# Performance work log

Hardware: AMD Instinct MI355X
Metric: run time of the kernel (lower is better)

The kernel has to match this reference:

```python
import jax, jax.numpy as jnp
import numpy as np

B, L, D, N_ITEMS, HEADS = 32, 1024, 1024, 50000, 2


def setup_inputs() -> dict:
    key = jax.random.key(0)
    ks = jax.random.split(key, 14)
    positives = jax.random.randint(ks[0], (B, L), 0, N_ITEMS)
    mask = jax.random.randint(ks[1], (B, L), 0, 2).astype(jnp.int32)
    s = 0.02
    item_emb = jax.random.normal(ks[2], (N_ITEMS + 1, D), jnp.float32) * s
    pos_emb = jax.random.normal(ks[3], (L, D), jnp.float32) * s
    Wz = jax.random.normal(ks[4], (L, L), jnp.float32) * s
    Wv = jax.random.normal(ks[5], (L, L), jnp.float32) * s
    Wq = jax.random.normal(ks[6], (L, L), jnp.float32) * s
    Wk = jax.random.normal(ks[7], (L, L), jnp.float32) * s
    gamma_q = jax.random.normal(ks[8], (HEADS, L), jnp.float32) * s
    beta_q = jnp.zeros((HEADS, L), jnp.float32)
    gamma_k = jax.random.normal(ks[9], (HEADS, L), jnp.float32) * s
    beta_k = jnp.zeros((HEADS, L), jnp.float32)
    sparse_w = jax.random.uniform(ks[10], (L, L), jnp.float32)
    return {"positives": positives, "mask": mask, "item_emb": item_emb,
            "pos_emb": pos_emb, "Wz": Wz, "Wv": Wv, "Wq": Wq, "Wk": Wk,
            "gamma_q": gamma_q, "beta_q": beta_q, "gamma_k": gamma_k,
            "beta_k": beta_k, "sparse_w": sparse_w}


def _merge_attn_masks(mask):
    # True == not allowed to attend
    pad = ~(mask.astype(bool))[:, None, :]                 # (B,1,L)
    future = jnp.triu(jnp.ones((L, L), bool), k=1)         # (L,L)
    merged = pad | future[None]                             # (B,L,L)
    diag = ~jnp.eye(L, dtype=bool)
    return diag[None] & merged                              # (B,L,L) bool


def reference(positives, mask, item_emb, pos_emb, Wz, Wv, Wq, Wk,
              gamma_q, beta_q, gamma_k, beta_k, sparse_w):
    attn_mask = _merge_attn_masks(mask)                     # (B,L,L) bool
    x = item_emb[positives] + pos_emb[None]                 # (B,L,D)
    # encoder
    z = jax.nn.silu(jnp.einsum('bld,ed->ble', x, Wz))       # (B,L,L-dim feats)
    zq = jnp.einsum('bld,ed->ble', z, Wq)
    zk = jnp.einsum('bld,ed->ble', z, Wk)
    q = zq * gamma_q[0] + beta_q[0]                         # head 0 only
    k = zk * gamma_k[0] + beta_k[0]
    a = jnp.einsum('bqd,bkd->bqk', q, k) + attn_mask.astype(q.dtype)
    a = (a * (~attn_mask).astype(a.dtype)) * sparse_w[None]
    a = jnp.square(jax.nn.relu(a)) / (L * D)
    v = jax.nn.silu(jnp.einsum('bld,ed->ble', x, Wv))       # (B,L,D)
    return jnp.einsum('bqk,bkd->bqd', a, v)                 # (B,L,D)
```

## Files before the change

### kernel.cpp

```cpp
#include <hip/hip_runtime.h>

#define L 1024
#define DD 1024
#define BATCH 32
#define M_TOTAL (BATCH * L)

typedef _Float16 f16;
typedef __attribute__((ext_vector_type(4))) _Float16 f16x4;
typedef __attribute__((ext_vector_type(8))) _Float16 f16x8;
typedef __attribute__((ext_vector_type(4))) float f32x4;

__device__ __forceinline__ void load16_lds(const void* g, void* l) {
  __builtin_amdgcn_global_load_lds(
      (const __attribute__((address_space(1))) unsigned int*)g,
      (__attribute__((address_space(3))) unsigned int*)l,
      16, 0, 0);
}


__global__ void gather_x_kernel(const int* __restrict__ positives,
                                const float* __restrict__ item_emb,
                                const float* __restrict__ pos_emb,
                                f16* __restrict__ x) {
  const int bl = blockIdx.x;
  const int lpos = bl & (L - 1);
  const int idx = positives[bl];
  const int d = threadIdx.x * 4;
  const float4 ie = *(const float4*)(item_emb + (size_t)idx * DD + d);
  const float4 pe = *(const float4*)(pos_emb + (size_t)lpos * DD + d);
  f16x4 h;
  h[0] = (f16)(ie.x + pe.x);
  h[1] = (f16)(ie.y + pe.y);
  h[2] = (f16)(ie.z + pe.z);
  h[3] = (f16)(ie.w + pe.w);
  *(f16x4*)(x + (size_t)bl * DD + d) = h;
}

__global__ void cast_w_kernel(const float* __restrict__ src, f16* __restrict__ dst) {
  const int i = (blockIdx.x * 256 + threadIdx.x) * 4;
  const float4 v = *(const float4*)(src + i);
  f16x4 h;
  h[0] = (f16)v.x; h[1] = (f16)v.y; h[2] = (f16)v.z; h[3] = (f16)v.w;
  *(f16x4*)(dst + i) = h;
}

__global__ void transpose_v_kernel(const unsigned short* __restrict__ vin,
                                   unsigned short* __restrict__ vout) {
  const int b = blockIdx.z;
  const unsigned short* in = vin + (size_t)b * L * DD;
  unsigned short* out = vout + (size_t)b * L * DD;
  const int r0 = blockIdx.x * 64, c0 = blockIdx.y * 64;
  __shared__ unsigned short t[64][65];
  const int tid = threadIdx.x;
  for (int c = tid; c < 1024; c += 256) {
    const int r = c >> 4, cc = (c & 15) * 4;
    const ushort4 vv = *(const ushort4*)(in + (size_t)(r0 + r) * DD + c0 + cc);
    t[r][cc] = vv.x; t[r][cc + 1] = vv.y; t[r][cc + 2] = vv.z; t[r][cc + 3] = vv.w;
  }
  __syncthreads();
  for (int c = tid; c < 1024; c += 256) {
    const int r = c >> 4, cc = (c & 15) * 4;
    ushort4 vv;
    vv.x = t[cc][r]; vv.y = t[cc + 1][r]; vv.z = t[cc + 2][r]; vv.w = t[cc + 3][r];
    *(ushort4*)(out + (size_t)(c0 + r) * L + r0 + cc) = vv;
  }
}


#define LDSOFF(d, mt, c, r) (((((d) * 2 + (mt)) * 8 + (c)) * 256 + (r)) * 8)

template <int EPI, int NTN>
__global__ __launch_bounds__(512, 2) void gemm256_kernel(
    const f16* __restrict__ A, const f16* __restrict__ B, f16* __restrict__ Cout,
    const size_t ldA, const size_t ldC,
    const float* __restrict__ g0, const float* __restrict__ b0,
    const float* __restrict__ g1, const float* __restrict__ b1, const float scale) {
  extern __shared__ f16 lds[];
  const int bid = blockIdx.x;
  const int cpx = gridDim.x >> 3;
  const int logical = (bid & 7) * cpx + (bid >> 3);
  const int mt = logical / NTN, nt = logical % NTN;
  const int tm0 = mt * 256, tn0 = nt * 256;
  const int tid = threadIdx.x;
  const int w = tid >> 6, l = tid & 63;
  const int wr = w >> 2, wc = w & 3;
  const int qd = l >> 4, mlo = l & 15;
  const int c1 = w >> 1, rbh = w & 1;
  const f16* Ag = A + (size_t)tm0 * ldA;
  const f16* Bg = B + (size_t)tn0 * 1024;

  auto stageA = [&](int dd, int h, int k0) {
    const int rb = h * 2 + rbh;
    load16_lds(Ag + (size_t)(rb * 64 + l) * ldA + k0 + c1 * 8,
               lds + LDSOFF(dd, 0, c1, rb * 64));
    load16_lds(Ag + (size_t)(rb * 64 + l) * ldA + k0 + (c1 + 4) * 8,
               lds + LDSOFF(dd, 0, c1 + 4, rb * 64));
  };
  auto stageB = [&](int dd, int h, int k0) {
    const int rb = h * 2 + rbh;
    load16_lds(Bg + (size_t)(rb * 64 + l) * 1024 + k0 + c1 * 8,
               lds + LDSOFF(dd, 1, c1, rb * 64));
    load16_lds(Bg + (size_t)(rb * 64 + l) * 1024 + k0 + (c1 + 4) * 8,
               lds + LDSOFF(dd, 1, c1 + 4, rb * 64));
  };

  f32x4 acc[8][4] = {};

  stageA(0, 0, 0); stageA(0, 1, 0); stageB(0, 0, 0); stageB(0, 1, 0);
  asm volatile("" ::: "memory");
  stageA(1, 0, 64); stageA(1, 1, 64); stageB(1, 0, 64); stageB(1, 1, 64);
  asm volatile("s_waitcnt vmcnt(8)" ::: "memory");
  __builtin_amdgcn_s_barrier();

#define LDA(mi, s) (*(const f16x8*)(lds + LDSOFF(d, 0, (s) * 4 + qd, wr * 128 + (mi) * 16 + mlo)))
#define LDB(ni, s) (*(const f16x8*)(lds + LDSOFF(d, 1, (s) * 4 + qd, wc * 64 + (ni) * 16 + mlo)))
#define MFMA16(a, b, c) __builtin_amdgcn_mfma_f32_16x16x32_f16(a, b, c, 0, 0, 0)

#pragma unroll 2
  for (int t = 0; t < 16; ++t) {
    const int d = t & 1;
    const int k2 = (t + 2) * 64;
    f16x8 a0[4][2], a1[4][2], bA[2][2], bB[2][2];
#pragma unroll
    for (int m = 0; m < 4; ++m) { a0[m][0] = LDA(m, 0); a0[m][1] = LDA(m, 1); }
#pragma unroll
    for (int n = 0; n < 2; ++n) { bA[n][0] = LDB(n, 0); bA[n][1] = LDB(n, 1); }
    __builtin_amdgcn_s_barrier();
    __builtin_amdgcn_s_setprio(1);
#pragma unroll
    for (int m = 0; m < 4; ++m)
#pragma unroll
      for (int n = 0; n < 2; ++n) {
        acc[m][n] = MFMA16(a0[m][0], bA[n][0], acc[m][n]);
        acc[m][n] = MFMA16(a0[m][1], bA[n][1], acc[m][n]);
      }
    __builtin_amdgcn_s_setprio(0);
    __builtin_amdgcn_s_barrier();
#pragma unroll
    for (int n = 0; n < 2; ++n) { bB[n][0] = LDB(n + 2, 0); bB[n][1] = LDB(n + 2, 1); }
    __builtin_amdgcn_s_barrier();
    __builtin_amdgcn_s_setprio(1);
#pragma unroll
    for (int m = 0; m < 4; ++m)
#pragma unroll
      for (int n = 0; n < 2; ++n) {
        acc[m][n + 2] = MFMA16(a0[m][0], bB[n][0], acc[m][n + 2]);
        acc[m][n + 2] = MFMA16(a0[m][1], bB[n][1], acc[m][n + 2]);
      }
    __builtin_amdgcn_s_setprio(0);
    __builtin_amdgcn_s_barrier();
#pragma unroll
    for (int m = 0; m < 4; ++m) { a1[m][0] = LDA(m + 4, 0); a1[m][1] = LDA(m + 4, 1); }
    if (t < 14) { stageB(d, 0, k2); stageB(d, 1, k2); }
    __builtin_amdgcn_s_barrier();
    __builtin_amdgcn_s_setprio(1);
#pragma unroll
    for (int m = 0; m < 4; ++m)
#pragma unroll
      for (int n = 0; n < 2; ++n) {
        acc[m + 4][n] = MFMA16(a1[m][0], bA[n][0], acc[m + 4][n]);
        acc[m + 4][n] = MFMA16(a1[m][1], bA[n][1], acc[m + 4][n]);
      }
    __builtin_amdgcn_s_setprio(0);
    __builtin_amdgcn_s_barrier();
    if (t < 14) { stageA(d, 0, k2); stageA(d, 1, k2); }
    __builtin_amdgcn_s_barrier();
    __builtin_amdgcn_s_setprio(1);
#pragma unroll
    for (int m = 0; m < 4; ++m)
#pragma unroll
      for (int n = 0; n < 2; ++n) {
        acc[m + 4][n + 2] = MFMA16(a1[m][0], bB[n][0], acc[m + 4][n + 2]);
        acc[m + 4][n + 2] = MFMA16(a1[m][1], bB[n][1], acc[m + 4][n + 2]);
      }
    __builtin_amdgcn_s_setprio(0);
    if (t < 14) {
      asm volatile("s_waitcnt vmcnt(8)" ::: "memory");
    } else if (t == 14) {
      asm volatile("s_waitcnt vmcnt(0)" ::: "memory");
    }
    __builtin_amdgcn_s_barrier();
  }

#pragma unroll
  for (int i = 0; i < 8; ++i) {
#pragma unroll
    for (int j = 0; j < 4; ++j) {
      const int gn = tn0 + wc * 64 + j * 16 + mlo;
      float gg = 1.0f, bb = 0.0f;
      if (EPI == 1) {
        gg = (gn < 1024) ? g0[gn] : g1[gn - 1024];
        bb = (gn < 1024) ? b0[gn] : b1[gn - 1024];
      }
#pragma unroll
      for (int r = 0; r < 4; ++r) {
        const int gm = tm0 + wr * 128 + i * 16 + qd * 4 + r;
        float y = acc[i][j][r];
        if (EPI == 0) {
          y = y / (1.0f + __expf(-y));
        } else {
          y = (y * gg + bb) * scale;
        }
        Cout[(size_t)gm * ldC + gn] = (f16)y;
      }
    }
  }
}

__global__ __launch_bounds__(256) void qk_kernel(
    const f16* __restrict__ QK,
    const int* __restrict__ mask, const float* __restrict__ sparse_w,
    f16* __restrict__ P) {
  const int qt = blockIdx.x, kt = blockIdx.y, b = blockIdx.z;
  if (kt * 2 > qt) return;
  const f16* A = QK + (size_t)b * L * 2048;
  const f16* B = QK + (size_t)b * L * 2048 + 1024;
  const int* mb = mask + b * L;
  f16* Pb = P + (size_t)b * L * L;
  __shared__ f16 As[4][64][8];
  __shared__ f16 Bs[4][128][8];
  const int tm0 = qt * 64, tn0 = kt * 128;
  const int tid = threadIdx.x;
  const int w = tid >> 6, l = tid & 63;
  const int wr = w >> 1, wc = w & 1;
  const int qd = l >> 4, mlo = l & 15;
  f32x4 acc[2][4] = {};
  for (int k0 = 0; k0 < L; k0 += 32) {
    load16_lds(A + (size_t)(tm0 + l) * 2048 + k0 + w * 8, &As[w][0][0]);
#pragma unroll
    for (int s = 0; s < 2; ++s)
      load16_lds(B + (size_t)(tn0 + s * 64 + l) * 2048 + k0 + w * 8, &Bs[w][s * 64][0]);
    __syncthreads();
    f16x8 af[2], bf[4];
#pragma unroll
    for (int i = 0; i < 2; ++i) af[i] = *(const f16x8*)&As[qd][wr * 32 + i * 16 + mlo][0];
#pragma unroll
    for (int j = 0; j < 4; ++j) bf[j] = *(const f16x8*)&Bs[qd][wc * 64 + j * 16 + mlo][0];
#pragma unroll
    for (int i = 0; i < 2; ++i)
#pragma unroll
      for (int j = 0; j < 4; ++j)
        acc[i][j] = __builtin_amdgcn_mfma_f32_16x16x32_f16(af[i], bf[j], acc[i][j], 0, 0, 0);
    __syncthreads();
  }
#pragma unroll
  for (int i = 0; i < 2; ++i) {
#pragma unroll
    for (int j = 0; j < 4; ++j) {
      const int gk = tn0 + wc * 64 + j * 16 + mlo;
      const int mk = mb[gk];
#pragma unroll
      for (int r = 0; r < 4; ++r) {
        const int gq = tm0 + wr * 32 + i * 16 + qd * 4 + r;
        float p = 0.0f;
        const bool blocked = (gk > gq) || ((gk != gq) && (mk == 0));
        if (!blocked) {
          p = acc[i][j][r] * sparse_w[(size_t)gq * L + gk];
          p = fmaxf(p, 0.0f);
          p = p * p;
        }
        Pb[(size_t)gq * L + gk] = (f16)p;
      }
    }
  }
}

__global__ __launch_bounds__(256) void pv_kernel(
    const f16* __restrict__ P, const f16* __restrict__ Vt, float* __restrict__ Out) {
  const int qt = blockIdx.x, nt = blockIdx.y, b = blockIdx.z;
  const f16* A = P + (size_t)b * L * L;
  const f16* B = Vt + (size_t)b * L * DD;
  float* outb = Out + (size_t)b * L * DD;
  const int kmax = (qt + 1) * 128;
  __shared__ f16 As[4][128][8];
  __shared__ f16 Bs[4][128][8];
  const int tm0 = qt * 128, tn0 = nt * 128;
  const int tid = threadIdx.x;
  const int w = tid >> 6, l = tid & 63;
  const int wr = w >> 1, wc = w & 1;
  const int qd = l >> 4, mlo = l & 15;
  f32x4 acc[4][4] = {};
  for (int k0 = 0; k0 < kmax; k0 += 32) {
#pragma unroll
    for (int s = 0; s < 2; ++s) {
      const int t = w * 2 + s;
      const int q = t >> 1, mh = t & 1;
      load16_lds(A + (size_t)(tm0 + mh * 64 + l) * L + k0 + q * 8, &As[q][mh * 64][0]);
      load16_lds(B + (size_t)(tn0 + mh * 64 + l) * L + k0 + q * 8, &Bs[q][mh * 64][0]);
    }
    __syncthreads();
    f16x8 af[4], bf[4];
#pragma unroll
    for (int i = 0; i < 4; ++i) af[i] = *(const f16x8*)&As[qd][wr * 64 + i * 16 + mlo][0];
#pragma unroll
    for (int j = 0; j < 4; ++j) bf[j] = *(const f16x8*)&Bs[qd][wc * 64 + j * 16 + mlo][0];
#pragma unroll
    for (int i = 0; i < 4; ++i)
#pragma unroll
      for (int j = 0; j < 4; ++j)
        acc[i][j] = __builtin_amdgcn_mfma_f32_16x16x32_f16(af[i], bf[j], acc[i][j], 0, 0, 0);
    __syncthreads();
  }
  const float fin = 5.421010862427522e-20f;
#pragma unroll
  for (int i = 0; i < 4; ++i) {
#pragma unroll
    for (int j = 0; j < 4; ++j) {
#pragma unroll
      for (int r = 0; r < 4; ++r) {
        const int gq = tm0 + wr * 64 + i * 16 + qd * 4 + r;
        const int gd = tn0 + wc * 64 + j * 16 + mlo;
        outb[(size_t)gq * DD + gd] = acc[i][j][r] * fin;
      }
    }
  }
}

extern "C" void kernel_launch(void* const* d_in, const int* in_sizes, int n_in,
                              void* d_out, int out_size, void* d_ws, size_t ws_size,
                              hipStream_t stream) {
  const int* positives = (const int*)d_in[0];
  const int* mask = (const int*)d_in[1];
  const float* item_emb = (const float*)d_in[2];
  const float* pos_emb = (const float*)d_in[3];
  const float* Wz = (const float*)d_in[4];
  const float* Wv = (const float*)d_in[5];
  const float* Wq = (const float*)d_in[6];
  const float* Wk = (const float*)d_in[7];
  const float* gamma_q = (const float*)d_in[8];
  const float* beta_q = (const float*)d_in[9];
  const float* gamma_k = (const float*)d_in[10];
  const float* beta_k = (const float*)d_in[11];
  const float* sparse_w = (const float*)d_in[12];
  float* out = (float*)d_out;

  char* ws = (char*)d_ws;
  const size_t MB = 1024 * 1024;
  f16* Wzh = (f16*)(ws + 0 * MB);
  f16* Wvh = (f16*)(ws + 2 * MB);
  f16* Wqkh = (f16*)(ws + 4 * MB);
  f16* bufZ = (f16*)(ws + 8 * MB);
  f16* bufV = (f16*)(ws + 72 * MB);
  f16* bufQK = (f16*)(ws + 136 * MB);
  f16* bufX = bufQK;

  static bool attr_set = false;
  if (!attr_set) {
    hipFuncSetAttribute(reinterpret_cast<const void*>(gemm256_kernel<0, 4>),
                        hipFuncAttributeMaxDynamicSharedMemorySize, 131072);
    hipFuncSetAttribute(reinterpret_cast<const void*>(gemm256_kernel<1, 8>),
                        hipFuncAttributeMaxDynamicSharedMemorySize, 131072);
    (void)hipGetLastError();
    attr_set = true;
  }

  cast_w_kernel<<<1024, 256, 0, stream>>>(Wz, Wzh);
  cast_w_kernel<<<1024, 256, 0, stream>>>(Wv, Wvh);
  cast_w_kernel<<<1024, 256, 0, stream>>>(Wq, Wqkh);
  cast_w_kernel<<<1024, 256, 0, stream>>>(Wk, Wqkh + 1024 * 1024);
  gather_x_kernel<<<M_TOTAL, 256, 0, stream>>>(positives, item_emb, pos_emb, bufX);

  gemm256_kernel<0, 4><<<512, 512, 131072, stream>>>(
      bufX, Wzh, bufZ, 1024, 1024, nullptr, nullptr, nullptr, nullptr, 1.0f);
  gemm256_kernel<0, 4><<<512, 512, 131072, stream>>>(
      bufX, Wvh, bufV, 1024, 1024, nullptr, nullptr, nullptr, nullptr, 1.0f);
  gemm256_kernel<1, 8><<<1024, 512, 131072, stream>>>(
      bufZ, Wqkh, bufQK, 1024, 2048, gamma_q, beta_q, gamma_k, beta_k, 2048.0f);
  const dim3 gt(16, 16, BATCH);
  transpose_v_kernel<<<gt, 256, 0, stream>>>((const unsigned short*)bufV, (unsigned short*)bufZ);
  const dim3 gqk(16, 8, BATCH);
  qk_kernel<<<gqk, 256, 0, stream>>>(bufQK, mask, sparse_w, bufV);
  const dim3 gpv(8, 8, BATCH);
  pv_kernel<<<gpv, 256, 0, stream>>>(bufV, bufZ, out);
}
```

Measured before the change: 1.132 ms.

## Route QK and PV attention GEMMs through shared 256x256 pipelined GEMM core

```diff
diff --git a/kernel.cpp b/kernel.cpp
--- a/kernel.cpp
+++ b/kernel.cpp
@@ -69,6 +69,112 @@
 
 #define LDSOFF(d, mt, c, r) (((((d) * 2 + (mt)) * 8 + (c)) * 256 + (r)) * 8)
 
+__device__ __forceinline__ void pipeline256(
+    const f16* __restrict__ Ag, const size_t ldA,
+    const f16* __restrict__ Bg, const size_t ldB,
+    f16* __restrict__ lds, f32x4 (&acc)[8][4],
+    const int tid, const int nkt) {
+  const int w = tid >> 6, l = tid & 63;
+  const int wr = w >> 2, wc = w & 3;
+  const int qd = l >> 4, mlo = l & 15;
+  const int c1 = w >> 1, rbh = w & 1;
+
+  auto stageA = [&](int dd, int h, int k0) {
+    const int rb = h * 2 + rbh;
+    load16_lds(Ag + (size_t)(rb * 64 + l) * ldA + k0 + c1 * 8,
+               lds + LDSOFF(dd, 0, c1, rb * 64));
+    load16_lds(Ag + (size_t)(rb * 64 + l) * ldA + k0 + (c1 + 4) * 8,
+               lds + LDSOFF(dd, 0, c1 + 4, rb * 64));
+  };
+  auto stageB = [&](int dd, int h, int k0) {
+    const int rb = h * 2 + rbh;
+    load16_lds(Bg + (size_t)(rb * 64 + l) * ldB + k0 + c1 * 8,
+               lds + LDSOFF(dd, 1, c1, rb * 64));
+    load16_lds(Bg + (size_t)(rb * 64 + l) * ldB + k0 + (c1 + 4) * 8,
+               lds + LDSOFF(dd, 1, c1 + 4, rb * 64));
+  };
+
+  stageA(0, 0, 0); stageA(0, 1, 0); stageB(0, 0, 0); stageB(0, 1, 0);
+  asm volatile("" ::: "memory");
+  stageA(1, 0, 64); stageA(1, 1, 64); stageB(1, 0, 64); stageB(1, 1, 64);
+  asm volatile("s_waitcnt vmcnt(8)" ::: "memory");
+  __builtin_amdgcn_s_barrier();
+
+#define LDA(mi, s) (*(const f16x8*)(lds + LDSOFF(d, 0, (s) * 4 + qd, wr * 128 + (mi) * 16 + mlo)))
+#define LDB(ni, s) (*(const f16x8*)(lds + LDSOFF(d, 1, (s) * 4 + qd, wc * 64 + (ni) * 16 + mlo)))
+#define MFMA16(a, b, c) __builtin_amdgcn_mfma_f32_16x16x32_f16(a, b, c, 0, 0, 0)
+
+#pragma unroll 2
+  for (int t = 0; t < nkt; ++t) {
+    const int d = t & 1;
+    const int k2 = (t + 2) * 64;
+    const bool more = (t < nkt - 2);
+    f16x8 a0[4][2], a1[4][2], bA[2][2], bB[2][2];
+#pragma unroll
+    for (int m = 0; m < 4; ++m) { a0[m][0] = LDA(m, 0); a0[m][1] = LDA(m, 1); }
+#pragma unroll
+    for (int n = 0; n < 2; ++n) { bA[n][0] = LDB(n, 0); bA[n][1] = LDB(n, 1); }
+    __builtin_amdgcn_s_barrier();
+    __builtin_amdgcn_s_setprio(1);
+#pragma unroll
+    for (int m = 0; m < 4; ++m)
+#pragma unroll
+      for (int n = 0; n < 2; ++n) {
+        acc[m][n] = MFMA16(a0[m][0], bA[n][0], acc[m][n]);
+        acc[m][n] = MFMA16(a0[m][1], bA[n][1], acc[m][n]);
+      }
+    __builtin_amdgcn_s_setprio(0);
+    __builtin_amdgcn_s_barrier();
+#pragma unroll
+    for (int n = 0; n < 2; ++n) { bB[n][0] = LDB(n + 2, 0); bB[n][1] = LDB(n + 2, 1); }
+    __builtin_amdgcn_s_barrier();
+    __builtin_amdgcn_s_setprio(1);
+#pragma unroll
+    for (int m = 0; m < 4; ++m)
+#pragma unroll
+      for (int n = 0; n < 2; ++n) {
+        acc[m][n + 2] = MFMA16(a0[m][0], bB[n][0], acc[m][n + 2]);
+        acc[m][n + 2] = MFMA16(a0[m][1], bB[n][1], acc[m][n + 2]);
+      }
+    __builtin_amdgcn_s_setprio(0);
+    __builtin_amdgcn_s_barrier();
+#pragma unroll
+    for (int m = 0; m < 4; ++m) { a1[m][0] = LDA(m + 4, 0); a1[m][1] = LDA(m + 4, 1); }
+    if (more) { stageB(d, 0, k2); stageB(d, 1, k2); }
+    __builtin_amdgcn_s_barrier();
+    __builtin_amdgcn_s_setprio(1);
+#pragma unroll
+    for (int m = 0; m < 4; ++m)
+#pragma unroll
+      for (int n = 0; n < 2; ++n) {
+        acc[m + 4][n] = MFMA16(a1[m][0], bA[n][0], acc[m + 4][n]);
+        acc[m + 4][n] = MFMA16(a1[m][1], bA[n][1], acc[m + 4][n]);
+      }
+    __builtin_amdgcn_s_setprio(0);
+    __builtin_amdgcn_s_barrier();
+    if (more) { stageA(d, 0, k2); stageA(d, 1, k2); }
+    __builtin_amdgcn_s_barrier();
+    __builtin_amdgcn_s_setprio(1);
+#pragma unroll
+    for (int m = 0; m < 4; ++m)
+#pragma unroll
+      for (int n = 0; n < 2; ++n) {
+        acc[m + 4][n + 2] = MFMA16(a1[m][0], bB[n][0], acc[m + 4][n + 2]);
+        acc[m + 4][n + 2] = MFMA16(a1[m][1], bB[n][1], acc[m + 4][n + 2]);
+      }
+    __builtin_amdgcn_s_setprio(0);
+    if (more) {
+      asm volatile("s_waitcnt vmcnt(8)" ::: "memory");
+    } else if (t == nkt - 2) {
+      asm volatile("s_waitcnt vmcnt(0)" ::: "memory");
+    }
+    __builtin_amdgcn_s_barrier();
+  }
+#undef LDA
+#undef LDB
+#undef MFMA16
+}
+
 template <int EPI, int NTN>
 __global__ __launch_bounds__(512, 2) void gemm256_kernel(
     const f16* __restrict__ A, const f16* __restrict__ B, f16* __restrict__ Cout,
@@ -82,106 +188,13 @@
   const int mt = logical / NTN, nt = logical % NTN;
   const int tm0 = mt * 256, tn0 = nt * 256;
   const int tid = threadIdx.x;
+
+  f32x4 acc[8][4] = {};
+  pipeline256(A + (size_t)tm0 * ldA, ldA, B + (size_t)tn0 * 1024, 1024, lds, acc, tid, 16);
+
   const int w = tid >> 6, l = tid & 63;
   const int wr = w >> 2, wc = w & 3;
   const int qd = l >> 4, mlo = l & 15;
-  const int c1 = w >> 1, rbh = w & 1;
-  const f16* Ag = A + (size_t)tm0 * ldA;
-  const f16* Bg = B + (size_t)tn0 * 1024;
-
-  auto stageA = [&](int dd, int h, int k0) {
-    const int rb = h * 2 + rbh;
-    load16_lds(Ag + (size_t)(rb * 64 + l) * ldA + k0 + c1 * 8,
-               lds + LDSOFF(dd, 0, c1, rb * 64));
-    load16_lds(Ag + (size_t)(rb * 64 + l) * ldA + k0 + (c1 + 4) * 8,
-               lds + LDSOFF(dd, 0, c1 + 4, rb * 64));
-  };
-  auto stageB = [&](int dd, int h, int k0) {
-    const int rb = h * 2 + rbh;
-    load16_lds(Bg + (size_t)(rb * 64 + l) * 1024 + k0 + c1 * 8,
-               lds + LDSOFF(dd, 1, c1, rb * 64));
-    load16_lds(Bg + (size_t)(rb * 64 + l) * 1024 + k0 + (c1 + 4) * 8,
-               lds + LDSOFF(dd, 1, c1 + 4, rb * 64));
-  };
-
-  f32x4 acc[8][4] = {};
-
-  stageA(0, 0, 0); stageA(0, 1, 0); stageB(0, 0, 0); stageB(0, 1, 0);
-  asm volatile("" ::: "memory");
-  stageA(1, 0, 64); stageA(1, 1, 64); stageB(1, 0, 64); stageB(1, 1, 64);
-  asm volatile("s_waitcnt vmcnt(8)" ::: "memory");
-  __builtin_amdgcn_s_barrier();
-
-#define LDA(mi, s) (*(const f16x8*)(lds + LDSOFF(d, 0, (s) * 4 + qd, wr * 128 + (mi) * 16 + mlo)))
-#define LDB(ni, s) (*(const f16x8*)(lds + LDSOFF(d, 1, (s) * 4 + qd, wc * 64 + (ni) * 16 + mlo)))
-#define MFMA16(a, b, c) __builtin_amdgcn_mfma_f32_16x16x32_f16(a, b, c, 0, 0, 0)
-
-#pragma unroll 2
-  for (int t = 0; t < 16; ++t) {
-    const int d = t & 1;
-    const int k2 = (t + 2) * 64;
-    f16x8 a0[4][2], a1[4][2], bA[2][2], bB[2][2];
-#pragma unroll
-    for (int m = 0; m < 4; ++m) { a0[m][0] = LDA(m, 0); a0[m][1] = LDA(m, 1); }
-#pragma unroll
-    for (int n = 0; n < 2; ++n) { bA[n][0] = LDB(n, 0); bA[n][1] = LDB(n, 1); }
-    __builtin_amdgcn_s_barrier();
-    __builtin_amdgcn_s_setprio(1);
-#pragma unroll
-    for (int m = 0; m < 4; ++m)
-#pragma unroll
-      for (int n = 0; n < 2; ++n) {
-        acc[m][n] = MFMA16(a0[m][0], bA[n][0], acc[m][n]);
-        acc[m][n] = MFMA16(a0[m][1], bA[n][1], acc[m][n]);
-      }
-    __builtin_amdgcn_s_setprio(0);
-    __builtin_amdgcn_s_barrier();
-#pragma unroll
-    for (int n = 0; n < 2; ++n) { bB[n][0] = LDB(n + 2, 0); bB[n][1] = LDB(n + 2, 1); }
-    __builtin_amdgcn_s_barrier();
-    __builtin_amdgcn_s_setprio(1);
-#pragma unroll
-    for (int m = 0; m < 4; ++m)
-#pragma unroll
-      for (int n = 0; n < 2; ++n) {
-        acc[m][n + 2] = MFMA16(a0[m][0], bB[n][0], acc[m][n + 2]);
-        acc[m][n + 2] = MFMA16(a0[m][1], bB[n][1], acc[m][n + 2]);
-      }
-    __builtin_amdgcn_s_setprio(0);
-    __builtin_amdgcn_s_barrier();
-#pragma unroll
-    for (int m = 0; m < 4; ++m) { a1[m][0] = LDA(m + 4, 0); a1[m][1] = LDA(m + 4, 1); }
-    if (t < 14) { stageB(d, 0, k2); stageB(d, 1, k2); }
-    __builtin_amdgcn_s_barrier();
-    __builtin_amdgcn_s_setprio(1);
-#pragma unroll
-    for (int m = 0; m < 4; ++m)
-#pragma unroll
-      for (int n = 0; n < 2; ++n) {
-        acc[m + 4][n] = MFMA16(a1[m][0], bA[n][0], acc[m + 4][n]);
-        acc[m + 4][n] = MFMA16(a1[m][1], bA[n][1], acc[m + 4][n]);
-      }
-    __builtin_amdgcn_s_setprio(0);
-    __builtin_amdgcn_s_barrier();
-    if (t < 14) { stageA(d, 0, k2); stageA(d, 1, k2); }
-    __builtin_amdgcn_s_barrier();
-    __builtin_amdgcn_s_setprio(1);
-#pragma unroll
-    for (int m = 0; m < 4; ++m)
-#pragma unroll
-      for (int n = 0; n < 2; ++n) {
-        acc[m + 4][n + 2] = MFMA16(a1[m][0], bB[n][0], acc[m + 4][n + 2]);
-        acc[m + 4][n + 2] = MFMA16(a1[m][1], bB[n][1], acc[m + 4][n + 2]);
-      }
-    __builtin_amdgcn_s_setprio(0);
-    if (t < 14) {
-      asm volatile("s_waitcnt vmcnt(8)" ::: "memory");
-    } else if (t == 14) {
-      asm volatile("s_waitcnt vmcnt(0)" ::: "memory");
-    }
-    __builtin_amdgcn_s_barrier();
-  }
-
 #pragma unroll
   for (int i = 0; i < 8; ++i) {
 #pragma unroll
@@ -207,51 +220,42 @@
   }
 }
 
-__global__ __launch_bounds__(256) void qk_kernel(
+__global__ __launch_bounds__(512, 2) void qk256_kernel(
     const f16* __restrict__ QK,
     const int* __restrict__ mask, const float* __restrict__ sparse_w,
     f16* __restrict__ P) {
-  const int qt = blockIdx.x, kt = blockIdx.y, b = blockIdx.z;
-  if (kt * 2 > qt) return;
-  const f16* A = QK + (size_t)b * L * 2048;
-  const f16* B = QK + (size_t)b * L * 2048 + 1024;
+  extern __shared__ f16 lds[];
+  const int bid = blockIdx.x;
+  const int logical = (bid & 7) * 40 + (bid >> 3);
+  const int b = logical / 10;
+  const int t10 = logical - b * 10;
+  int mt, nt;
+  if (t10 == 0)      { mt = 0; nt = 0; }
+  else if (t10 <= 2) { mt = 1; nt = t10 - 1; }
+  else if (t10 <= 5) { mt = 2; nt = t10 - 3; }
+  else               { mt = 3; nt = t10 - 6; }
+  const int tm0 = mt * 256, tn0 = nt * 256;
+  const f16* Ag = QK + (size_t)b * L * 2048 + (size_t)tm0 * 2048;
+  const f16* Bg = QK + (size_t)b * L * 2048 + 1024 + (size_t)tn0 * 2048;
+  const int tid = threadIdx.x;
+
+  f32x4 acc[8][4] = {};
+  pipeline256(Ag, 2048, Bg, 2048, lds, acc, tid, 16);
+
+  const int w = tid >> 6, l = tid & 63;
+  const int wr = w >> 2, wc = w & 3;
+  const int qd = l >> 4, mlo = l & 15;
   const int* mb = mask + b * L;
   f16* Pb = P + (size_t)b * L * L;
-  __shared__ f16 As[4][64][8];
-  __shared__ f16 Bs[4][128][8];
-  const int tm0 = qt * 64, tn0 = kt * 128;
-  const int tid = threadIdx.x;
-  const int w = tid >> 6, l = tid & 63;
-  const int wr = w >> 1, wc = w & 1;
-  const int qd = l >> 4, mlo = l & 15;
-  f32x4 acc[2][4] = {};
-  for (int k0 = 0; k0 < L; k0 += 32) {
-    load16_lds(A + (size_t)(tm0 + l) * 2048 + k0 + w * 8, &As[w][0][0]);
-#pragma unroll
-    for (int s = 0; s < 2; ++s)
-      load16_lds(B + (size_t)(tn0 + s * 64 + l) * 2048 + k0 + w * 8, &Bs[w][s * 64][0]);
-    __syncthreads();
-    f16x8 af[2], bf[4];
-#pragma unroll
-    for (int i = 0; i < 2; ++i) af[i] = *(const f16x8*)&As[qd][wr * 32 + i * 16 + mlo][0];
-#pragma unroll
-    for (int j = 0; j < 4; ++j) bf[j] = *(const f16x8*)&Bs[qd][wc * 64 + j * 16 + mlo][0];
-#pragma unroll
-    for (int i = 0; i < 2; ++i)
-#pragma unroll
-      for (int j = 0; j < 4; ++j)
-        acc[i][j] = __builtin_amdgcn_mfma_f32_16x16x32_f16(af[i], bf[j], acc[i][j], 0, 0, 0);
-    __syncthreads();
-  }
-#pragma unroll
-  for (int i = 0; i < 2; ++i) {
+#pragma unroll
+  for (int i = 0; i < 8; ++i) {
 #pragma unroll
     for (int j = 0; j < 4; ++j) {
       const int gk = tn0 + wc * 64 + j * 16 + mlo;
       const int mk = mb[gk];
 #pragma unroll
       for (int r = 0; r < 4; ++r) {
-        const int gq = tm0 + wr * 32 + i * 16 + qd * 4 + r;
+        const int gq = tm0 + wr * 128 + i * 16 + qd * 4 + r;
         float p = 0.0f;
         const bool blocked = (gk > gq) || ((gk != gq) && (mk == 0));
         if (!blocked) {
@@ -265,50 +269,34 @@
   }
 }
 
-__global__ __launch_bounds__(256) void pv_kernel(
+__global__ __launch_bounds__(512, 2) void pv256_kernel(
     const f16* __restrict__ P, const f16* __restrict__ Vt, float* __restrict__ Out) {
-  const int qt = blockIdx.x, nt = blockIdx.y, b = blockIdx.z;
-  const f16* A = P + (size_t)b * L * L;
-  const f16* B = Vt + (size_t)b * L * DD;
+  extern __shared__ f16 lds[];
+  const int bid = blockIdx.x;
+  const int logical = (bid & 7) * 64 + (bid >> 3);
+  const int b = logical >> 4;
+  const int tile = logical & 15;
+  const int mt = tile >> 2, nt = tile & 3;
+  const int tm0 = mt * 256, tn0 = nt * 256;
+  const f16* Ag = P + (size_t)b * L * L + (size_t)tm0 * L;
+  const f16* Bg = Vt + (size_t)b * L * DD + (size_t)tn0 * L;
+  const int tid = threadIdx.x;
+
+  f32x4 acc[8][4] = {};
+  pipeline256(Ag, L, Bg, L, lds, acc, tid, (mt + 1) * 4);
+
+  const int w = tid >> 6, l = tid & 63;
+  const int wr = w >> 2, wc = w & 3;
+  const int qd = l >> 4, mlo = l & 15;
   float* outb = Out + (size_t)b * L * DD;
-  const int kmax = (qt + 1) * 128;
-  __shared__ f16 As[4][128][8];
-  __shared__ f16 Bs[4][128][8];
-  const int tm0 = qt * 128, tn0 = nt * 128;
-  const int tid = threadIdx.x;
-  const int w = tid >> 6, l = tid & 63;
-  const int wr = w >> 1, wc = w & 1;
-  const int qd = l >> 4, mlo = l & 15;
-  f32x4 acc[4][4] = {};
-  for (int k0 = 0; k0 < kmax; k0 += 32) {
-#pragma unroll
-    for (int s = 0; s < 2; ++s) {
-      const int t = w * 2 + s;
-      const int q = t >> 1, mh = t & 1;
-      load16_lds(A + (size_t)(tm0 + mh * 64 + l) * L + k0 + q * 8, &As[q][mh * 64][0]);
-      load16_lds(B + (size_t)(tn0 + mh * 64 + l) * L + k0 + q * 8, &Bs[q][mh * 64][0]);
-    }
-    __syncthreads();
-    f16x8 af[4], bf[4];
-#pragma unroll
-    for (int i = 0; i < 4; ++i) af[i] = *(const f16x8*)&As[qd][wr * 64 + i * 16 + mlo][0];
-#pragma unroll
-    for (int j = 0; j < 4; ++j) bf[j] = *(const f16x8*)&Bs[qd][wc * 64 + j * 16 + mlo][0];
-#pragma unroll
-    for (int i = 0; i < 4; ++i)
-#pragma unroll
-      for (int j = 0; j < 4; ++j)
-        acc[i][j] = __builtin_amdgcn_mfma_f32_16x16x32_f16(af[i], bf[j], acc[i][j], 0, 0, 0);
-    __syncthreads();
-  }
   const float fin = 5.421010862427522e-20f;
 #pragma unroll
-  for (int i = 0; i < 4; ++i) {
+  for (int i = 0; i < 8; ++i) {
 #pragma unroll
     for (int j = 0; j < 4; ++j) {
 #pragma unroll
       for (int r = 0; r < 4; ++r) {
-        const int gq = tm0 + wr * 64 + i * 16 + qd * 4 + r;
+        const int gq = tm0 + wr * 128 + i * 16 + qd * 4 + r;
         const int gd = tn0 + wc * 64 + j * 16 + mlo;
         outb[(size_t)gq * DD + gd] = acc[i][j][r] * fin;
       }
@@ -350,6 +338,10 @@
                         hipFuncAttributeMaxDynamicSharedMemorySize, 131072);
     hipFuncSetAttribute(reinterpret_cast<const void*>(gemm256_kernel<1, 8>),
                         hipFuncAttributeMaxDynamicSharedMemorySize, 131072);
+    hipFuncSetAttribute(reinterpret_cast<const void*>(qk256_kernel),
+                        hipFuncAttributeMaxDynamicSharedMemorySize, 131072);
+    hipFuncSetAttribute(reinterpret_cast<const void*>(pv256_kernel),
+                        hipFuncAttributeMaxDynamicSharedMemorySize, 131072);
     (void)hipGetLastError();
     attr_set = true;
   }
@@ -368,8 +360,6 @@
       bufZ, Wqkh, bufQK, 1024, 2048, gamma_q, beta_q, gamma_k, beta_k, 2048.0f);
   const dim3 gt(16, 16, BATCH);
   transpose_v_kernel<<<gt, 256, 0, stream>>>((const unsigned short*)bufV, (unsigned short*)bufZ);
-  const dim3 gqk(16, 8, BATCH);
-  qk_kernel<<<gqk, 256, 0, stream>>>(bufQK, mask, sparse_w, bufV);
-  const dim3 gpv(8, 8, BATCH);
-  pv_kernel<<<gpv, 256, 0, stream>>>(bufV, bufZ, out);
-}
+  qk256_kernel<<<320, 512, 131072, stream>>>(bufQK, mask, sparse_w, bufV);
+  pv256_kernel<<<512, 512, 131072, stream>>>(bufV, bufZ, out);
+}
```

Measured after the change: 1.015 ms. 10.3% less time.
